# Optimization experiments

Measured on AMD Instinct MI355X. Metric: run time of the kernel, lower is better.

Reference implementation:

```python
import jax, jax.numpy as jnp
import numpy as np

B, S, E, H = 8, 1024, 1024, 16
DK = E // H  # = n_wires = 64


def setup_inputs() -> dict:
    key = jax.random.key(0)
    k1, k2, k3 = jax.random.split(key, 3)
    x = jax.random.normal(k1, (B, S, E), dtype=jnp.float32)
    # trainable per-wire RX angles (shared across tokens and heads, as in QLayer)
    theta = jax.random.normal(k2, (DK,), dtype=jnp.float32)
    # combine_heads: nn.Linear(E, E, bias=False) -> weight [E, E], y = x @ W.T
    W_combine = (jax.random.normal(k3, (E, E), dtype=jnp.float32) / np.float32(np.sqrt(E)))
    return {"x": x, "theta": theta, "W_combine": W_combine}


def reference(x, theta, W_combine):
    # Quantum projection: per wire, RX(x_i) then RX(theta_i) on |0>, measure PauliZ.
    # RX(a)RX(b) = RX(a+b); <Z> of RX(a)|0> = cos(a)  =>  proj = cos(x + theta).
    b, s, e = x.shape
    xh = x.reshape(b, s, H, DK)            # [B, S, H, DK]
    proj = jnp.cos(xh + theta)             # product-state circuit, fully vectorized
    qkv = proj.transpose(0, 2, 1, 3)       # [B, H, S, DK]; q = k = v = proj

    scale = jnp.float32(1.0 / np.sqrt(DK))
    scores = jnp.einsum('bhqd,bhkd->bhqk', qkv, qkv) * scale  # [B, H, S, S]
    attn = jax.nn.softmax(scores, axis=-1)  # dropout disabled (eval / p=0)
    out = jnp.einsum('bhqk,bhkd->bhqd', attn, qkv)            # [B, H, S, DK]
    out = out.transpose(0, 2, 1, 3).reshape(b, s, e)          # [B, S, E]
    return out @ W_combine.T
```

## Files before the change

kernel.cpp:

```cpp
#include <hip/hip_runtime.h>
#include <hip/hip_bf16.h>
#include <stdint.h>

typedef float  f32x4   __attribute__((ext_vector_type(4)));
typedef float  f32x16  __attribute__((ext_vector_type(16)));
typedef __bf16 bf16x8  __attribute__((ext_vector_type(8)));
typedef __bf16 bf16x4  __attribute__((ext_vector_type(4)));

static constexpr int NB = 8, NS = 1024, NE = 1024, NH = 16;

#define MFMA16(a, b, c) __builtin_amdgcn_mfma_f32_16x16x32_bf16((a), (b), (c), 0, 0, 0)
#define MFMA32(a, b, c) __builtin_amdgcn_mfma_f32_32x32x16_bf16((a), (b), (c), 0, 0, 0)

__device__ __forceinline__ void gload_lds16(const void* g, void* l) {
    __builtin_amdgcn_global_load_lds(
        (const __attribute__((address_space(1))) void*)g,
        (__attribute__((address_space(3))) void*)l, 16, 0, 0);
}

__device__ __forceinline__ uint32_t cvt_pk_bf16(float lo, float hi) {
    uint32_t r;
    asm("v_cvt_pk_bf16_f32 %0, %1, %2" : "=v"(r) : "v"(lo), "v"(hi));
    return r;
}
__device__ __forceinline__ void pl32swap(uint32_t& a, uint32_t& b) {
    asm volatile("v_permlane32_swap_b32 %0, %1" : "+v"(a), "+v"(b));
}
__device__ __forceinline__ float exp2_raw(float x) {
    float r;
    asm("v_exp_f32 %0, %1" : "=v"(r) : "v"(x));
    return r;
}

__global__ __launch_bounds__(256) void k_proj(const float* __restrict__ x,
                                              const float* __restrict__ theta,
                                              __bf16* __restrict__ proj,
                                              __bf16* __restrict__ projT,
                                              const float* __restrict__ W,
                                              __bf16* __restrict__ Wb) {
    __shared__ float sm[64][65];
    const int bid = blockIdx.x;
    const int t   = threadIdx.x;

    if (bid >= 2048) {
        const int i = ((bid - 2048) * 256 + t) * 4;
        float4 v = *(const float4*)(W + i);
        bf16x4 o = {(__bf16)v.x, (__bf16)v.y, (__bf16)v.z, (__bf16)v.w};
        *(bf16x4*)(Wb + i) = o;
        return;
    }

    const int bh   = bid >> 4;
    const int st0  = (bid & 15) << 6;
    const int b    = bh >> 4, h = bh & 15;
    const int srow = t >> 2;
    const int j4   = t & 3;

    const float* xrow = x + ((size_t)(b * NS + st0 + srow)) * NE + h * 64;
    __bf16* prow = proj + ((size_t)bh * NS + st0 + srow) * 64;

#pragma unroll
    for (int k = 0; k < 4; ++k) {
        const int d = k * 16 + j4 * 4;
        float4 xv = *(const float4*)(xrow + d);
        float4 tv = *(const float4*)(theta + d);
        float c0 = __cosf(xv.x + tv.x);
        float c1 = __cosf(xv.y + tv.y);
        float c2 = __cosf(xv.z + tv.z);
        float c3 = __cosf(xv.w + tv.w);
        bf16x4 pv = {(__bf16)c0, (__bf16)c1, (__bf16)c2, (__bf16)c3};
        *(bf16x4*)(prow + d) = pv;
        sm[d + 0][srow] = c0;
        sm[d + 1][srow] = c1;
        sm[d + 2][srow] = c2;
        sm[d + 3][srow] = c3;
    }
    __syncthreads();

    const int drow = t >> 2;
    bf16x8 o0, o1;
#pragma unroll
    for (int i = 0; i < 8; ++i) {
        o0[i] = (__bf16)sm[drow][j4 * 16 + i];
        o1[i] = (__bf16)sm[drow][j4 * 16 + 8 + i];
    }
    __bf16* dst = projT + ((size_t)bh * 64 + drow) * NS + st0 + j4 * 16;
    *(bf16x8*)dst = o0;
    *(bf16x8*)(dst + 8) = o1;
}

__global__ __launch_bounds__(256, 2) void k_attn(const __bf16* __restrict__ proj,
                                                 const __bf16* __restrict__ projT,
                                                 __bf16* __restrict__ attn_out) {
    __shared__ __align__(16) char smem[32768];
    __bf16* const smK0 = (__bf16*)(smem);
    __bf16* const smV0 = (__bf16*)(smem + 8192);
    __bf16* const smK1 = (__bf16*)(smem + 16384);
    __bf16* const smV1 = (__bf16*)(smem + 24576);

    const int bid  = blockIdx.x;
    const int bh   = (bid & 7) + 8 * ((bid >> 3) & 15);
    const int qblk = bid >> 7;
    const int t    = threadIdx.x;
    const int w    = t >> 6;
    const int lane = t & 63;
    const int hi   = lane >> 5;
    const int l5   = lane & 31;
    const int l7   = l5 & 7;
    const int qw   = qblk * 256 + w * 64;
    const int b    = bh >> 4, h = bh & 15;

    const __bf16* P  = proj  + (size_t)bh * NS * 64;
    const __bf16* PT = projT + (size_t)bh * 64 * NS;

    const float csc = 0.18033688f;

    bf16x8 bq[2][4];
#pragma unroll
    for (int q01 = 0; q01 < 2; ++q01)
#pragma unroll
        for (int d = 0; d < 4; ++d)
            bq[q01][d] = *(const bf16x8*)(P + (size_t)(qw + q01 * 32 + l5) * 64 + d * 16 + hi * 8);

    int roff[4];
#pragma unroll
    for (int d = 0; d < 4; ++d) roff[d] = l5 * 64 + ((d * 2 + hi) ^ l7) * 8;

    const int srow  = t >> 3;
    const int sjsrc = (t & 7) ^ (srow & 7);
    char* const dK0 = (char*)smK0 + t * 16;
    char* const dV0 = (char*)smV0 + t * 16;
    char* const dK1 = (char*)smK1 + t * 16;
    char* const dV1 = (char*)smV1 + t * 16;

#define STAGE(kvoff, dk, dv)                                                           \
    do {                                                                               \
        gload_lds16(P  + (size_t)((kvoff) + srow)      * 64 + sjsrc * 8, (dk));        \
        gload_lds16(P  + (size_t)((kvoff) + 32 + srow) * 64 + sjsrc * 8, (dk) + 4096); \
        gload_lds16(PT + (size_t)srow        * NS + (kvoff) + sjsrc * 8, (dv));        \
        gload_lds16(PT + (size_t)(32 + srow) * NS + (kvoff) + sjsrc * 8, (dv) + 4096); \
    } while (0)

    f32x16 acc0[2], acc1[2];
#pragma unroll
    for (int dt = 0; dt < 2; ++dt) {
        acc0[dt] = (f32x16){0.f,0.f,0.f,0.f,0.f,0.f,0.f,0.f,0.f,0.f,0.f,0.f,0.f,0.f,0.f,0.f};
        acc1[dt] = (f32x16){0.f,0.f,0.f,0.f,0.f,0.f,0.f,0.f,0.f,0.f,0.f,0.f,0.f,0.f,0.f,0.f};
    }
    float rs0 = 0.f, rs1 = 0.f;

    auto computeTile = [&](const __bf16* kB, const __bf16* vB) {
#pragma unroll
        for (int kt = 0; kt < 2; ++kt) {
            bf16x8 ak[4];
#pragma unroll
            for (int d = 0; d < 4; ++d)
                ak[d] = *(const bf16x8*)(kB + roff[d] + kt * 2048);

            f32x16 st0 = (f32x16){0.f,0.f,0.f,0.f,0.f,0.f,0.f,0.f,0.f,0.f,0.f,0.f,0.f,0.f,0.f,0.f};
            f32x16 st1 = (f32x16){0.f,0.f,0.f,0.f,0.f,0.f,0.f,0.f,0.f,0.f,0.f,0.f,0.f,0.f,0.f,0.f};
            __builtin_amdgcn_s_setprio(1);
#pragma unroll
            for (int d = 0; d < 4; ++d) {
                st0 = MFMA32(ak[d], bq[0][d], st0);
                st1 = MFMA32(ak[d], bq[1][d], st1);
            }
            __builtin_amdgcn_s_setprio(0);

            uint32_t c0[8], c1[8];
            {
                float p[16];
#pragma unroll
                for (int r = 0; r < 16; ++r) p[r] = exp2_raw(st0[r] * csc);
                rs0 += (((p[0] + p[1]) + (p[2] + p[3])) + ((p[4] + p[5]) + (p[6] + p[7]))) +
                       (((p[8] + p[9]) + (p[10] + p[11])) + ((p[12] + p[13]) + (p[14] + p[15])));
#pragma unroll
                for (int j = 0; j < 8; ++j) c0[j] = cvt_pk_bf16(p[2 * j], p[2 * j + 1]);
            }
            {
                float p[16];
#pragma unroll
                for (int r = 0; r < 16; ++r) p[r] = exp2_raw(st1[r] * csc);
                rs1 += (((p[0] + p[1]) + (p[2] + p[3])) + ((p[4] + p[5]) + (p[6] + p[7]))) +
                       (((p[8] + p[9]) + (p[10] + p[11])) + ((p[12] + p[13]) + (p[14] + p[15])));
#pragma unroll
                for (int j = 0; j < 8; ++j) c1[j] = cvt_pk_bf16(p[2 * j], p[2 * j + 1]);
            }
            pl32swap(c0[0], c0[2]); pl32swap(c0[1], c0[3]);
            pl32swap(c0[4], c0[6]); pl32swap(c0[5], c0[7]);
            pl32swap(c1[0], c1[2]); pl32swap(c1[1], c1[3]);
            pl32swap(c1[4], c1[6]); pl32swap(c1[5], c1[7]);

#pragma unroll
            for (int half = 0; half < 2; ++half) {
                const int ks = kt * 2 + half;
                union U4 { uint32_t u[4]; bf16x8 v; };
                U4 f0, f1;
#pragma unroll
                for (int j = 0; j < 4; ++j) {
                    f0.u[j] = c0[half * 4 + j];
                    f1.u[j] = c1[half * 4 + j];
                }
                __builtin_amdgcn_s_setprio(1);
#pragma unroll
                for (int dt = 0; dt < 2; ++dt) {
                    bf16x8 av = *(const bf16x8*)(vB + roff[ks] + dt * 2048);
                    acc0[dt] = MFMA32(av, f0.v, acc0[dt]);
                    acc1[dt] = MFMA32(av, f1.v, acc1[dt]);
                }
                __builtin_amdgcn_s_setprio(0);
            }
        }
    };

    STAGE(0, dK0, dV0);
    __syncthreads();

#pragma unroll 1
    for (int it2 = 0; it2 < 8; ++it2) {
        STAGE((2 * it2 + 1) * 64, dK1, dV1);
        computeTile(smK0, smV0);
        __syncthreads();
        if (it2 < 7) STAGE((2 * it2 + 2) * 64, dK0, dV0);
        computeTile(smK1, smV1);
        __syncthreads();
    }
#undef STAGE

    float* const epw = (float*)smem + w * (32 * 33);
    const int orow = lane >> 1;
    const int ohalf = lane & 1;

#pragma unroll
    for (int q01 = 0; q01 < 2; ++q01) {
        float rs = (q01 == 0) ? rs0 : rs1;
        rs += __shfl_xor(rs, 32);
        const float inv = 1.0f / rs;
#pragma unroll
        for (int dt = 0; dt < 2; ++dt) {
            const f32x16 a = (q01 == 0) ? acc0[dt] : acc1[dt];
#pragma unroll
            for (int r = 0; r < 16; ++r)
                epw[l5 * 33 + (r & 3) + 8 * (r >> 2) + 4 * hi] = a[r] * inv;
            bf16x8 o0, o1;
#pragma unroll
            for (int i = 0; i < 8; ++i) {
                o0[i] = (__bf16)(epw[orow * 33 + ohalf * 16 + i]);
                o1[i] = (__bf16)(epw[orow * 33 + ohalf * 16 + 8 + i]);
            }
            __bf16* dst = attn_out +
                ((size_t)b * NS + qblk * 256 + w * 64 + q01 * 32 + orow) * NE +
                h * 64 + dt * 32 + ohalf * 16;
            *(bf16x8*)dst = o0;
            *(bf16x8*)(dst + 8) = o1;
        }
    }
}

__global__ __launch_bounds__(256, 4) void k_gemm(const __bf16* __restrict__ A,
                                                 const __bf16* __restrict__ Bw,
                                                 float* __restrict__ C) {
    constexpr int K = 1024, N = 1024;
    __shared__ __align__(16) __bf16 As[2][64 * 32];
    __shared__ __align__(16) __bf16 Bs[2][128 * 32];

    const int t = threadIdx.x;
    const int lane = t & 63, w = t >> 6;
    const int g = lane >> 4, c = lane & 15;
    const int wr = w >> 1, wc = w & 1;
    const size_t row0 = (size_t)blockIdx.y * 64;
    const size_t col0 = (size_t)blockIdx.x * 128;

    const __bf16* Ag = A  + row0 * K;
    const __bf16* Bg = Bw + col0 * K;

    const int srow = t >> 2;
    const int sj   = (t & 3) ^ ((srow >> 1) & 3);

#define GSTAGE(kb, buf)                                                          \
    do {                                                                         \
        gload_lds16(Ag + (size_t)srow * K + (kb) + sj * 8,                       \
                    (char*)&As[buf][0] + t * 16);                                \
        gload_lds16(Bg + (size_t)srow * K + (kb) + sj * 8,                       \
                    (char*)&Bs[buf][0] + t * 16);                                \
        gload_lds16(Bg + (size_t)(64 + srow) * K + (kb) + sj * 8,                \
                    (char*)&Bs[buf][0] + 4096 + t * 16);                         \
    } while (0)

    f32x4 acc[2][4];
#pragma unroll
    for (int m = 0; m < 2; ++m)
#pragma unroll
        for (int n = 0; n < 4; ++n) acc[m][n] = (f32x4){0.f, 0.f, 0.f, 0.f};

    auto computeBuf = [&](int buf) {
        bf16x8 a[2], bfr[4];
#pragma unroll
        for (int m = 0; m < 2; ++m) {
            const int row = wr * 32 + m * 16 + c;
            a[m] = *(const bf16x8*)(&As[buf][row * 32 + (g ^ ((row >> 1) & 3)) * 8]);
        }
#pragma unroll
        for (int n = 0; n < 4; ++n) {
            const int row = wc * 64 + n * 16 + c;
            bfr[n] = *(const bf16x8*)(&Bs[buf][row * 32 + (g ^ ((row >> 1) & 3)) * 8]);
        }
        __builtin_amdgcn_s_setprio(1);
#pragma unroll
        for (int m = 0; m < 2; ++m)
#pragma unroll
            for (int n = 0; n < 4; ++n) acc[m][n] = MFMA16(a[m], bfr[n], acc[m][n]);
        __builtin_amdgcn_s_setprio(0);
    };

    GSTAGE(0, 0);
    __syncthreads();

#pragma unroll 1
    for (int kt = 0; kt < 16; ++kt) {
        GSTAGE(kt * 64 + 32, 1);
        computeBuf(0);
        __syncthreads();
        if (kt < 15) GSTAGE(kt * 64 + 64, 0);
        computeBuf(1);
        __syncthreads();
    }
#undef GSTAGE

#pragma unroll
    for (int m = 0; m < 2; ++m)
#pragma unroll
        for (int n = 0; n < 4; ++n)
#pragma unroll
            for (int r = 0; r < 4; ++r)
                C[(row0 + wr * 32 + m * 16 + 4 * g + r) * N + col0 + wc * 64 + n * 16 + c] =
                    acc[m][n][r];
}

extern "C" void kernel_launch(void* const* d_in, const int* in_sizes, int n_in,
                              void* d_out, int out_size, void* d_ws, size_t ws_size,
                              hipStream_t stream) {
    const float* x     = (const float*)d_in[0];
    const float* theta = (const float*)d_in[1];
    const float* W     = (const float*)d_in[2];
    float* out = (float*)d_out;

    char* ws = (char*)d_ws;
    __bf16* proj  = (__bf16*)(ws);
    __bf16* projT = (__bf16*)(ws + 16777216);
    __bf16* Wb    = (__bf16*)(ws + 33554432);
    __bf16* ao    = (__bf16*)(ws + 35651584);

    k_proj<<<NB * NH * (NS / 64) + (NE * NE / 4) / 256, 256, 0, stream>>>(
        x, theta, proj, projT, W, Wb);
    k_attn<<<NB * NH * 4, 256, 0, stream>>>(proj, projT, ao);
    dim3 gg(NE / 128, NB * NS / 64);
    k_gemm<<<gg, 256, 0, stream>>>(ao, Wb, out);
}
```

Before: 86.80 us.

## Use 128x128 GEMM tiles with intra-block split-K across two warp groups

The output-projection GEMM moves from 64x128 tiles with 256 threads to 128x128 tiles with 512 threads. The two groups of four waves each handle half of every 64-wide K step, then combine their partial sums through shared memory before the store. The grid is transposed so consecutive blocks walk along rows of A, and LDS offsets are precomputed. The aim is more data reuse per loaded tile and more MFMA work per barrier, at the cost of 64KB of LDS, a reduction epilogue, and fewer resident blocks.

```diff
diff --git a/kernel.cpp b/kernel.cpp
--- a/kernel.cpp
+++ b/kernel.cpp
@@ -257,59 +257,71 @@
     }
 }
 
-__global__ __launch_bounds__(256, 4) void k_gemm(const __bf16* __restrict__ A,
+__global__ __launch_bounds__(512, 2) void k_gemm(const __bf16* __restrict__ A,
                                                  const __bf16* __restrict__ Bw,
                                                  float* __restrict__ C) {
     constexpr int K = 1024, N = 1024;
-    __shared__ __align__(16) __bf16 As[2][64 * 32];
-    __shared__ __align__(16) __bf16 Bs[2][128 * 32];
+    __shared__ __align__(16) char smem[65536];
 
     const int t = threadIdx.x;
     const int lane = t & 63, w = t >> 6;
+    const int kh = w >> 2, q = w & 3;
+    const int wr = q >> 1, wc = q & 1;
     const int g = lane >> 4, c = lane & 15;
-    const int wr = w >> 1, wc = w & 1;
-    const size_t row0 = (size_t)blockIdx.y * 64;
-    const size_t col0 = (size_t)blockIdx.x * 128;
-
-    const __bf16* Ag = A  + row0 * K;
-    const __bf16* Bg = Bw + col0 * K;
-
-    const int srow = t >> 2;
-    const int sj   = (t & 3) ^ ((srow >> 1) & 3);
-
-#define GSTAGE(kb, buf)                                                          \
-    do {                                                                         \
-        gload_lds16(Ag + (size_t)srow * K + (kb) + sj * 8,                       \
-                    (char*)&As[buf][0] + t * 16);                                \
-        gload_lds16(Bg + (size_t)srow * K + (kb) + sj * 8,                       \
-                    (char*)&Bs[buf][0] + t * 16);                                \
-        gload_lds16(Bg + (size_t)(64 + srow) * K + (kb) + sj * 8,                \
-                    (char*)&Bs[buf][0] + 4096 + t * 16);                         \
+    const size_t row0 = (size_t)blockIdx.x * 128;
+    const size_t col0 = (size_t)blockIdx.y * 128;
+
+    const int ts   = t & 255;
+    const int sh   = t >> 8;
+    const int srow = ts >> 2;
+    const int sj   = (ts & 3) ^ ((srow >> 1) & 3);
+
+    const __bf16* Ag = A  + row0 * K + sh * 512;
+    const __bf16* Bg = Bw + col0 * K + sh * 512;
+
+    char* const aD[2] = {smem + sh * 8192,         smem + 16384 + sh * 8192};
+    char* const bD[2] = {smem + 32768 + sh * 8192, smem + 49152 + sh * 8192};
+    const char* const aR[2] = {smem + kh * 8192,         smem + 16384 + kh * 8192};
+    const char* const bR[2] = {smem + 32768 + kh * 8192, smem + 49152 + kh * 8192};
+
+#define GSTAGE(kt, buf)                                                                   \
+    do {                                                                                  \
+        gload_lds16(Ag + (size_t)srow * K + (kt) * 32 + sj * 8, aD[buf] + ts * 16);       \
+        gload_lds16(Ag + (size_t)(64 + srow) * K + (kt) * 32 + sj * 8,                    \
+                    aD[buf] + 4096 + ts * 16);                                            \
+        gload_lds16(Bg + (size_t)srow * K + (kt) * 32 + sj * 8, bD[buf] + ts * 16);       \
+        gload_lds16(Bg + (size_t)(64 + srow) * K + (kt) * 32 + sj * 8,                    \
+                    bD[buf] + 4096 + ts * 16);                                            \
     } while (0)
 
-    f32x4 acc[2][4];
-#pragma unroll
-    for (int m = 0; m < 2; ++m)
+    int aro[4], bro[4];
+#pragma unroll
+    for (int m = 0; m < 4; ++m) {
+        const int ra = wr * 64 + m * 16 + c;
+        aro[m] = ra * 32 + (g ^ ((ra >> 1) & 3)) * 8;
+        const int rb = wc * 64 + m * 16 + c;
+        bro[m] = rb * 32 + (g ^ ((rb >> 1) & 3)) * 8;
+    }
+
+    f32x4 acc[4][4];
+#pragma unroll
+    for (int m = 0; m < 4; ++m)
 #pragma unroll
         for (int n = 0; n < 4; ++n) acc[m][n] = (f32x4){0.f, 0.f, 0.f, 0.f};
 
     auto computeBuf = [&](int buf) {
-        bf16x8 a[2], bfr[4];
-#pragma unroll
-        for (int m = 0; m < 2; ++m) {
-            const int row = wr * 32 + m * 16 + c;
-            a[m] = *(const bf16x8*)(&As[buf][row * 32 + (g ^ ((row >> 1) & 3)) * 8]);
-        }
-#pragma unroll
-        for (int n = 0; n < 4; ++n) {
-            const int row = wc * 64 + n * 16 + c;
-            bfr[n] = *(const bf16x8*)(&Bs[buf][row * 32 + (g ^ ((row >> 1) & 3)) * 8]);
-        }
+        bf16x8 a[4], bb[4];
+#pragma unroll
+        for (int m = 0; m < 4; ++m)
+            a[m] = *(const bf16x8*)((const __bf16*)aR[buf] + aro[m]);
+#pragma unroll
+        for (int n = 0; n < 4; ++n)
+            bb[n] = *(const bf16x8*)((const __bf16*)bR[buf] + bro[n]);
         __builtin_amdgcn_s_setprio(1);
 #pragma unroll
-        for (int m = 0; m < 2; ++m)
-#pragma unroll
-            for (int n = 0; n < 4; ++n) acc[m][n] = MFMA16(a[m], bfr[n], acc[m][n]);
+        for (int m = 0; m < 4; ++m)
+#pragma unroll
+            for (int n = 0; n < 4; ++n) acc[m][n] = MFMA16(a[m], bb[n], acc[m][n]);
         __builtin_amdgcn_s_setprio(0);
     };
 
@@ -317,24 +329,42 @@
     __syncthreads();
 
 #pragma unroll 1
-    for (int kt = 0; kt < 16; ++kt) {
-        GSTAGE(kt * 64 + 32, 1);
+    for (int kt2 = 0; kt2 < 8; ++kt2) {
+        GSTAGE(2 * kt2 + 1, 1);
         computeBuf(0);
         __syncthreads();
-        if (kt < 15) GSTAGE(kt * 64 + 64, 0);
+        if (kt2 < 7) GSTAGE(2 * kt2 + 2, 0);
         computeBuf(1);
         __syncthreads();
     }
 #undef GSTAGE
 
-#pragma unroll
-    for (int m = 0; m < 2; ++m)
-#pragma unroll
-        for (int n = 0; n < 4; ++n)
-#pragma unroll
-            for (int r = 0; r < 4; ++r)
-                C[(row0 + wr * 32 + m * 16 + 4 * g + r) * N + col0 + wc * 64 + n * 16 + c] =
-                    acc[m][n][r];
+    float* const dmp = (float*)smem;
+    if (kh == 1) {
+#pragma unroll
+        for (int m = 0; m < 4; ++m)
+#pragma unroll
+            for (int n = 0; n < 4; ++n)
+                *(f32x4*)(dmp + q * 4096 + (m * 4 + n) * 256 + lane * 4) = acc[m][n];
+    }
+    __syncthreads();
+    if (kh == 0) {
+#pragma unroll
+        for (int m = 0; m < 4; ++m)
+#pragma unroll
+            for (int n = 0; n < 4; ++n) {
+                f32x4 v = *(const f32x4*)(dmp + q * 4096 + (m * 4 + n) * 256 + lane * 4);
+                acc[m][n] += v;
+            }
+#pragma unroll
+        for (int m = 0; m < 4; ++m)
+#pragma unroll
+            for (int n = 0; n < 4; ++n)
+#pragma unroll
+                for (int r = 0; r < 4; ++r)
+                    C[(row0 + wr * 64 + m * 16 + 4 * g + r) * N +
+                      col0 + wc * 64 + n * 16 + c] = acc[m][n][r];
+    }
 }
 
 extern "C" void kernel_launch(void* const* d_in, const int* in_sizes, int n_in,
@@ -354,6 +384,6 @@
     k_proj<<<NB * NH * (NS / 64) + (NE * NE / 4) / 256, 256, 0, stream>>>(
         x, theta, proj, projT, W, Wb);
     k_attn<<<NB * NH * 4, 256, 0, stream>>>(proj, projT, ao);
-    dim3 gg(NE / 128, NB * NS / 64);
-    k_gemm<<<gg, 256, 0, stream>>>(ao, Wb, out);
-}
+    dim3 gg(NB * NS / 128, NE / 128);
+    k_gemm<<<gg, 512, 0, stream>>>(ao, Wb, out);
+}
```

Result: faster. 79.74 us (-8.1%).
